# Kernel optimization log

Measured on AMD Instinct MI355X. Metric: run time of the kernel, lower is better.

The kernel has to match this reference:

```python
import jax, jax.numpy as jnp
import numpy as np

N = 50000
E = 800000
IN_DIM = 128
HID = 64


def _glorot(key, shape):
    fan_in, fan_out = shape[0], shape[-1]
    lim = jnp.sqrt(6.0 / (fan_in + fan_out))
    return jax.random.uniform(key, shape, jnp.float32, -lim, lim)


def setup_inputs() -> dict:
    key = jax.random.key(0)
    ks = jax.random.split(key, 12)
    x = jax.random.normal(ks[0], (N, IN_DIM), jnp.float32)
    edge_index = jax.random.randint(ks[1], (2, E), 0, N, jnp.int64)
    return {
        "x": x,
        "edge_index": edge_index,
        # GATConv 1: in=128 -> 64 per head, 4 heads (concat -> 256)
        "W1": _glorot(ks[2], (IN_DIM, 4 * HID)),
        "a_src1": _glorot(ks[3], (4, HID)),
        "a_dst1": _glorot(ks[4], (4, HID)),
        "b1": jnp.zeros((4 * HID,), jnp.float32),
        # GATConv 2: in=256 -> 64, 1 head
        "W2": _glorot(ks[5], (4 * HID, HID)),
        "a_src2": _glorot(ks[6], (1, HID)),
        "a_dst2": _glorot(ks[7], (1, HID)),
        "b2": jnp.zeros((HID,), jnp.float32),
        # classifier 64 -> 32 -> 2
        "W3": _glorot(ks[8], (HID, 32)),
        "b3": jnp.zeros((32,), jnp.float32),
        "W4": _glorot(ks[9], (32, 2)),
        "b4": jnp.zeros((2,), jnp.float32),
    }


def _gat_layer(x, edge_index, W, a_src, a_dst, b, heads, out_ch):
    """PyG-style GATConv (add_self_loops=True, negative_slope=0.2, concat)."""
    n = x.shape[0]
    loop = jnp.arange(n, dtype=edge_index.dtype)
    src = jnp.concatenate([edge_index[0], loop])  # [E+N]
    dst = jnp.concatenate([edge_index[1], loop])
    h = (x @ W).reshape(n, heads, out_ch)  # [N,H,C]
    as_ = jnp.sum(h * a_src[None], axis=-1)  # [N,H]
    ad_ = jnp.sum(h * a_dst[None], axis=-1)  # [N,H]
    e = jax.nn.leaky_relu(as_[src] + ad_[dst], negative_slope=0.2)  # [E+N,H]
    # segment softmax over destination nodes
    m = jax.ops.segment_max(e, dst, num_segments=n)  # [N,H]
    ex = jnp.exp(e - m[dst])
    s = jax.ops.segment_sum(ex, dst, num_segments=n)
    alpha = ex / (s[dst] + 1e-16)  # [E+N,H]
    msg = h[src] * alpha[:, :, None]  # [E+N,H,C]
    out = jax.ops.segment_sum(msg, dst, num_segments=n)  # [N,H,C]
    return out.reshape(n, heads * out_ch) + b


def reference(x, edge_index, W1, a_src1, a_dst1, b1, W2, a_src2, a_dst2, b2, W3, b3, W4, b4):
    h = jax.nn.elu(_gat_layer(x, edge_index, W1, a_src1, a_dst1, b1, heads=4, out_ch=HID))
    h = jax.nn.elu(_gat_layer(h, edge_index, W2, a_src2, a_dst2, b2, heads=1, out_ch=HID))
    h = jax.nn.relu(h @ W3 + b3)
    return h @ W4 + b4  # [N, 2] logits
```

## Files before the change

kernel.cpp:

```cpp
#include <hip/hip_runtime.h>
#include <math.h>

#define NNODES 50000
#define NEDGES 800000
#define CAP 128
#define SB 832

typedef __attribute__((ext_vector_type(8))) short bfrag8;
typedef __attribute__((ext_vector_type(4))) float f32x4;

__device__ __forceinline__ unsigned short f2bf(float f) {
    unsigned b = __float_as_uint(f);
    b += 0x7fffu + ((b >> 16) & 1u);
    return (unsigned short)(b >> 16);
}
__device__ __forceinline__ float bf_lo(unsigned u) { return __uint_as_float(u << 16); }
__device__ __forceinline__ float bf_hi(unsigned u) { return __uint_as_float(u & 0xffff0000u); }

__device__ __forceinline__ void pack_one(const float* W, unsigned short* Wp, int K, int NC,
                                         int idx) {
    int k = idx / NC, n = idx % NC;
    int kf = k >> 5, q = (k >> 3) & 3, j = k & 7;
    Wp[((((size_t)n * (K >> 5) + kf) * 4 + q) << 3) + j] = f2bf(W[idx]);
}

__global__ void prep_kernel(const float* __restrict__ x, unsigned short* __restrict__ xb,
                            const float* __restrict__ W1, unsigned short* __restrict__ W1p,
                            const float* __restrict__ W2, unsigned short* __restrict__ W2p,
                            int* __restrict__ cnt, int ncvt4, int n) {
    int idx = blockIdx.x * blockDim.x + threadIdx.x;
    if (idx < ncvt4) {
        float4 v = *(const float4*)&x[idx * 4];
        ushort4 s;
        s.x = f2bf(v.x); s.y = f2bf(v.y); s.z = f2bf(v.z); s.w = f2bf(v.w);
        *(ushort4*)&xb[idx * 4] = s;
    }
    if (idx < 128 * 256) pack_one(W1, W1p, 128, 256, idx);
    if (idx < 256 * 64) pack_one(W2, W2p, 256, 64, idx);
    if (idx < n) cnt[idx] = 0;
}

template <int K, int H>
__device__ __forceinline__ void gemm_dev(const unsigned short* __restrict__ Ab,
                                         const unsigned short* __restrict__ Bp,
                                         const float* __restrict__ a_src,
                                         const float* __restrict__ a_dst,
                                         unsigned short* __restrict__ Cb,
                                         float* __restrict__ as_, float* __restrict__ ad_,
                                         int M, int bid) {
    constexpr int KF = K / 32;
    constexpr int NC = H * 64;
    int wave = threadIdx.x >> 6, lane = threadIdx.x & 63;
    int m0 = (bid * 4 + wave) * 16;
    if (m0 >= M) return;
    int quad = lane >> 4, l16 = lane & 15;
    int row = m0 + l16;

    bfrag8 a[KF];
    const unsigned short* arow = Ab + (size_t)row * K + quad * 8;
#pragma unroll
    for (int f = 0; f < KF; f++) a[f] = *(const bfrag8*)(arow + f * 32);

    float ps[4] = {0.f, 0.f, 0.f, 0.f};
    float pd[4] = {0.f, 0.f, 0.f, 0.f};
#pragma unroll
    for (int nt = 0; nt < NC / 16; nt++) {
        f32x4 acc = {0.f, 0.f, 0.f, 0.f};
        const unsigned short* bp = Bp + (((size_t)(nt * 16 + l16) * KF) * 4 + quad) * 8;
#pragma unroll
        for (int f = 0; f < KF; f++) {
            bfrag8 bfr = *(const bfrag8*)(bp + (size_t)f * 32);
            acc = __builtin_amdgcn_mfma_f32_16x16x32_bf16(a[f], bfr, acc, 0, 0, 0);
        }
        int col = nt * 16 + l16;
        float avs = a_src[col], avd = a_dst[col];
#pragma unroll
        for (int r = 0; r < 4; r++) {
            ps[r] = fmaf(acc[r], avs, ps[r]);
            pd[r] = fmaf(acc[r], avd, pd[r]);
            unsigned pk = (unsigned)f2bf(acc[r]) |
                          ((unsigned)f2bf(__shfl_down(acc[r], 1)) << 16);
            if (!(l16 & 1))
                *(unsigned*)&Cb[(size_t)(m0 + quad * 4 + r) * NC + nt * 16 + l16] = pk;
        }
        if ((nt & 3) == 3) {
            int head = nt >> 2;
#pragma unroll
            for (int off = 1; off < 16; off <<= 1) {
#pragma unroll
                for (int r = 0; r < 4; r++) {
                    ps[r] += __shfl_xor(ps[r], off);
                    pd[r] += __shfl_xor(pd[r], off);
                }
            }
            if (l16 == 0) {
#pragma unroll
                for (int r = 0; r < 4; r++) {
                    as_[(size_t)(m0 + quad * 4 + r) * H + head] = ps[r];
                    ad_[(size_t)(m0 + quad * 4 + r) * H + head] = pd[r];
                }
            }
#pragma unroll
            for (int r = 0; r < 4; r++) { ps[r] = 0.f; pd[r] = 0.f; }
        }
    }
}

__global__ __launch_bounds__(256) void gemm1_scatter(
    const unsigned short* __restrict__ xb, const unsigned short* __restrict__ W1p,
    const float* __restrict__ a_src1, const float* __restrict__ a_dst1,
    unsigned short* __restrict__ h1b, float* __restrict__ as1, float* __restrict__ ad1,
    const int* __restrict__ ei, int* __restrict__ cnt, unsigned short* __restrict__ bucket,
    int M, int nE, int nT) {
    if ((int)blockIdx.x < SB) {
        int p = blockIdx.x & 7;
        int q = blockIdx.x >> 3;
        const int NQ = SB / 8;
        for (int idx = q * 256 + threadIdx.x; idx < nT; idx += NQ * 256) {
            int dst = (idx < nE) ? ei[nE + idx] : idx - nE;
            if ((dst & 7) != p) continue;
            int src = (idx < nE) ? ei[idx] : dst;
            int slot = atomicAdd(&cnt[dst], 1);
            if (slot < CAP) bucket[(size_t)dst * CAP + slot] = (unsigned short)src;
        }
    } else {
        gemm_dev<128, 4>(xb, W1p, a_src1, a_dst1, h1b, as1, ad1, M, blockIdx.x - SB);
    }
}

__global__ __launch_bounds__(256) void gemm2_kernel(
    const unsigned short* __restrict__ Ab, const unsigned short* __restrict__ Bp,
    const float* __restrict__ a_src, const float* __restrict__ a_dst,
    unsigned short* __restrict__ Cb, float* __restrict__ as_, float* __restrict__ ad_,
    int M) {
    gemm_dev<256, 1>(Ab, Bp, a_src, a_dst, Cb, as_, ad_, M, blockIdx.x);
}

__global__ void node_agg4(const int* __restrict__ cnt, const unsigned short* __restrict__ bucket,
                          const float* __restrict__ as_, const float* __restrict__ ad_,
                          const unsigned short* __restrict__ hb, const float* __restrict__ b,
                          unsigned short* __restrict__ outb, int n) {
    __shared__ float alf[4][64][4];
    __shared__ int srs[4][64];
    int w = threadIdx.x >> 6;
    int node = blockIdx.x * 4 + w;
    int lane = threadIdx.x & 63;
    if (node >= n) return;
    int cntAll = cnt[node];
    if (cntAll > CAP) cntAll = CAP;
    const unsigned short* bkt = bucket + (size_t)node * CAP;
    int cnt0 = cntAll < 64 ? cntAll : 64;
    bool v0 = lane < cnt0;
    int half = lane >> 5;
    int hl = lane & 31;
    int head = hl >> 3;
    int ch0 = hl * 8;

    float4 adv = *(const float4*)&ad_[node * 4];
    float adn[4] = {adv.x, adv.y, adv.z, adv.w};

    int src0 = bkt[v0 ? lane : 0];
    float4 asv = *(const float4*)&as_[src0 * 4];
    float x0[4];
    {
        float e0 = asv.x + adn[0], e1 = asv.y + adn[1];
        float e2 = asv.z + adn[2], e3 = asv.w + adn[3];
        e0 = e0 > 0.f ? e0 : 0.2f * e0;
        e1 = e1 > 0.f ? e1 : 0.2f * e1;
        e2 = e2 > 0.f ? e2 : 0.2f * e2;
        e3 = e3 > 0.f ? e3 : 0.2f * e3;
        x0[0] = v0 ? __expf(e0) : 0.f;
        x0[1] = v0 ? __expf(e1) : 0.f;
        x0[2] = v0 ? __expf(e2) : 0.f;
        x0[3] = v0 ? __expf(e3) : 0.f;
    }
    bool hv2 = false;
    int src2 = 0;
    float x2[4] = {0.f, 0.f, 0.f, 0.f};
    if (cntAll > 64) {
        int i2 = 64 + lane;
        hv2 = i2 < cntAll;
        src2 = bkt[hv2 ? i2 : 0];
        float4 a2 = *(const float4*)&as_[src2 * 4];
        float t0 = a2.x + adn[0], t1 = a2.y + adn[1];
        float t2 = a2.z + adn[2], t3 = a2.w + adn[3];
        t0 = t0 > 0.f ? t0 : 0.2f * t0;
        t1 = t1 > 0.f ? t1 : 0.2f * t1;
        t2 = t2 > 0.f ? t2 : 0.2f * t2;
        t3 = t3 > 0.f ? t3 : 0.2f * t3;
        x2[0] = hv2 ? __expf(t0) : 0.f;
        x2[1] = hv2 ? __expf(t1) : 0.f;
        x2[2] = hv2 ? __expf(t2) : 0.f;
        x2[3] = hv2 ? __expf(t3) : 0.f;
    }
    srs[w][lane] = src0;
    *(float4*)&alf[w][lane][0] = make_float4(x0[0], x0[1], x0[2], x0[3]);

    float acc[8];
#pragma unroll
    for (int k = 0; k < 8; k++) acc[k] = 0.f;

    int iters = (cnt0 + 1) >> 1;
    int iters4 = (iters + 3) & ~3;

#define LD4(vk, ak, t)                                              \
    {                                                               \
        int e_ = 2 * (t) + half;                                    \
        int s_ = srs[w][e_];                                        \
        ak = alf[w][e_][head];                                      \
        vk = *(const uint4*)&hb[(size_t)s_ * 256 + ch0];            \
    }
#define FMA8(ak, vk)                                                \
    {                                                               \
        acc[0] = fmaf(ak, bf_lo(vk.x), acc[0]);                     \
        acc[1] = fmaf(ak, bf_hi(vk.x), acc[1]);                     \
        acc[2] = fmaf(ak, bf_lo(vk.y), acc[2]);                     \
        acc[3] = fmaf(ak, bf_hi(vk.y), acc[3]);                     \
        acc[4] = fmaf(ak, bf_lo(vk.z), acc[4]);                     \
        acc[5] = fmaf(ak, bf_hi(vk.z), acc[5]);                     \
        acc[6] = fmaf(ak, bf_lo(vk.w), acc[6]);                     \
        acc[7] = fmaf(ak, bf_hi(vk.w), acc[7]);                     \
    }

    uint4 q0, q1, q2, q3;
    float a0, a1, a2, a3;
    LD4(q0, a0, 0) LD4(q1, a1, 1) LD4(q2, a2, 2) LD4(q3, a3, 3)
    int c = 0;
    for (; c < iters4 - 4; c += 4) {
        FMA8(a0, q0) LD4(q0, a0, c + 4)
        FMA8(a1, q1) LD4(q1, a1, c + 5)
        FMA8(a2, q2) LD4(q2, a2, c + 6)
        FMA8(a3, q3) LD4(q3, a3, c + 7)
    }
    FMA8(a0, q0) FMA8(a1, q1) FMA8(a2, q2) FMA8(a3, q3)

    if (cntAll > 64) {
        srs[w][lane] = src2;
        *(float4*)&alf[w][lane][0] = make_float4(x2[0], x2[1], x2[2], x2[3]);
        int c2 = cntAll - 64;
        for (int j = 0; j < c2; j += 2) {
            int e_ = j + half;
            int s_ = srs[w][e_];
            float al = alf[w][e_][head];
            uint4 v = *(const uint4*)&hb[(size_t)s_ * 256 + ch0];
            FMA8(al, v)
        }
    }
    float sl[4];
#pragma unroll
    for (int h = 0; h < 4; h++) sl[h] = x0[h] + x2[h];
#pragma unroll
    for (int off = 32; off > 0; off >>= 1) {
#pragma unroll
        for (int h = 0; h < 4; h++) sl[h] += __shfl_xor(sl[h], off);
    }
    float inv_h = 1.f / (sl[head] + 1e-16f);

#pragma unroll
    for (int k = 0; k < 8; k++) acc[k] += __shfl_down(acc[k], 32);
    if (half == 0) {
        float4 b0 = *(const float4*)&b[ch0];
        float4 b1 = *(const float4*)&b[ch0 + 4];
        float o[8] = {fmaf(acc[0], inv_h, b0.x), fmaf(acc[1], inv_h, b0.y),
                      fmaf(acc[2], inv_h, b0.z), fmaf(acc[3], inv_h, b0.w),
                      fmaf(acc[4], inv_h, b1.x), fmaf(acc[5], inv_h, b1.y),
                      fmaf(acc[6], inv_h, b1.z), fmaf(acc[7], inv_h, b1.w)};
#pragma unroll
        for (int k = 0; k < 8; k++) o[k] = o[k] > 0.f ? o[k] : __expf(o[k]) - 1.f;
        uint4 p;
        p.x = f2bf(o[0]) | ((unsigned)f2bf(o[1]) << 16);
        p.y = f2bf(o[2]) | ((unsigned)f2bf(o[3]) << 16);
        p.z = f2bf(o[4]) | ((unsigned)f2bf(o[5]) << 16);
        p.w = f2bf(o[6]) | ((unsigned)f2bf(o[7]) << 16);
        *(uint4*)&outb[(size_t)node * 256 + ch0] = p;
    }
#undef LD4
#undef FMA8
}

__global__ void node_agg1_cls(const int* __restrict__ cnt,
                              const unsigned short* __restrict__ bucket,
                              const float* __restrict__ as_, const float* __restrict__ ad_,
                              const unsigned short* __restrict__ hb,
                              const float* __restrict__ b2v,
                              const float* __restrict__ W3, const float* __restrict__ b3,
                              const float* __restrict__ W4, const float* __restrict__ b4,
                              float* __restrict__ out, int n) {
    __shared__ float alf[4][64];
    __shared__ int srs[4][64];
    __shared__ float w3s[2048];
    __shared__ float w4s[64], b3s[32], b4s[2];
    __shared__ float zrow[4][64];
    __shared__ float hrow[4][32];
    int tid = threadIdx.x;
    int w = tid >> 6;
    int lane = tid & 63;
#pragma unroll
    for (int i = 0; i < 8; i++) w3s[i * 256 + tid] = W3[i * 256 + tid];
    if (tid < 64) w4s[tid] = W4[tid];
    if (tid < 32) b3s[tid] = b3[tid];
    if (tid < 2) b4s[tid] = b4[tid];
    __syncthreads();

    int node = blockIdx.x * 4 + w;
    if (node >= n) return;
    int cntAll = cnt[node];
    if (cntAll > CAP) cntAll = CAP;
    const unsigned short* bkt = bucket + (size_t)node * CAP;
    int cnt0 = cntAll < 64 ? cntAll : 64;
    bool v0 = lane < cnt0;
    int q = lane >> 4;
    int ql = lane & 15;
    int ch0 = ql * 4;

    float adn = ad_[node];
    int src0 = bkt[v0 ? lane : 0];
    float ev = as_[src0] + adn;
    ev = ev > 0.f ? ev : 0.2f * ev;
    float x0 = v0 ? __expf(ev) : 0.f;

    bool hv2 = false;
    int src2 = 0;
    float x2 = 0.f;
    if (cntAll > 64) {
        int i2 = 64 + lane;
        hv2 = i2 < cntAll;
        src2 = bkt[hv2 ? i2 : 0];
        float t = as_[src2] + adn;
        t = t > 0.f ? t : 0.2f * t;
        x2 = hv2 ? __expf(t) : 0.f;
    }
    srs[w][lane] = src0;
    alf[w][lane] = x0;

    float acc[4] = {0.f, 0.f, 0.f, 0.f};
    int iters = (cnt0 + 3) >> 2;
    int iters4 = (iters + 3) & ~3;

#define LD2(vk, ak, t)                                              \
    {                                                               \
        int e_ = 4 * (t) + q;                                       \
        int s_ = srs[w][e_];                                        \
        ak = alf[w][e_];                                            \
        vk = *(const uint2*)&hb[(size_t)s_ * 64 + ch0];             \
    }
#define FMA4(ak, vk)                                                \
    {                                                               \
        acc[0] = fmaf(ak, bf_lo(vk.x), acc[0]);                     \
        acc[1] = fmaf(ak, bf_hi(vk.x), acc[1]);                     \
        acc[2] = fmaf(ak, bf_lo(vk.y), acc[2]);                     \
        acc[3] = fmaf(ak, bf_hi(vk.y), acc[3]);                     \
    }

    uint2 q0, q1, q2, q3;
    float a0, a1, a2, a3;
    LD2(q0, a0, 0) LD2(q1, a1, 1) LD2(q2, a2, 2) LD2(q3, a3, 3)
    int c = 0;
    for (; c < iters4 - 4; c += 4) {
        FMA4(a0, q0) LD2(q0, a0, c + 4)
        FMA4(a1, q1) LD2(q1, a1, c + 5)
        FMA4(a2, q2) LD2(q2, a2, c + 6)
        FMA4(a3, q3) LD2(q3, a3, c + 7)
    }
    FMA4(a0, q0) FMA4(a1, q1) FMA4(a2, q2) FMA4(a3, q3)

    if (cntAll > 64) {
        srs[w][lane] = src2;
        alf[w][lane] = x2;
        int c2 = cntAll - 64;
        for (int j = 0; j < c2; j += 4) {
            int e_ = j + q;
            int s_ = srs[w][e_];
            float al = alf[w][e_];
            uint2 v = *(const uint2*)&hb[(size_t)s_ * 64 + ch0];
            FMA4(al, v)
        }
    }
    float sl = x0 + x2;
#pragma unroll
    for (int off = 32; off > 0; off >>= 1) sl += __shfl_xor(sl, off);
    float inv_s = 1.f / (sl + 1e-16f);

#pragma unroll
    for (int k = 0; k < 4; k++) {
        acc[k] += __shfl_down(acc[k], 32);
        acc[k] += __shfl_down(acc[k], 16);
    }
    if (q == 0) {
        float4 bv = *(const float4*)&b2v[ch0];
        float o0 = fmaf(acc[0], inv_s, bv.x), o1 = fmaf(acc[1], inv_s, bv.y);
        float o2 = fmaf(acc[2], inv_s, bv.z), o3 = fmaf(acc[3], inv_s, bv.w);
        zrow[w][ch0 + 0] = o0 > 0.f ? o0 : __expf(o0) - 1.f;
        zrow[w][ch0 + 1] = o1 > 0.f ? o1 : __expf(o1) - 1.f;
        zrow[w][ch0 + 2] = o2 > 0.f ? o2 : __expf(o2) - 1.f;
        zrow[w][ch0 + 3] = o3 > 0.f ? o3 : __expf(o3) - 1.f;
    }
    {
        int p = lane & 1, j = lane >> 1;
        float partial = 0.f;
#pragma unroll
        for (int i = 0; i < 32; i++) {
            int k = p * 32 + i;
            partial = fmaf(zrow[w][k], w3s[k * 32 + j], partial);
        }
        partial += __shfl_down(partial, 1);
        if (p == 0) {
            float hv = partial + b3s[j];
            hrow[w][j] = hv > 0.f ? hv : 0.f;
        }
    }
    if (lane < 2) {
        float o = b4s[lane];
#pragma unroll
        for (int j = 0; j < 32; j++) o = fmaf(hrow[w][j], w4s[j * 2 + lane], o);
        out[(size_t)node * 2 + lane] = o;
    }
#undef LD2
#undef FMA4
}

extern "C" void kernel_launch(void* const* d_in, const int* in_sizes, int n_in,
                              void* d_out, int out_size, void* d_ws, size_t ws_size,
                              hipStream_t stream) {
    const float* x      = (const float*)d_in[0];
    const int*   ei     = (const int*)d_in[1];
    const float* W1     = (const float*)d_in[2];
    const float* a_src1 = (const float*)d_in[3];
    const float* a_dst1 = (const float*)d_in[4];
    const float* b1     = (const float*)d_in[5];
    const float* W2     = (const float*)d_in[6];
    const float* a_src2 = (const float*)d_in[7];
    const float* a_dst2 = (const float*)d_in[8];
    const float* b2     = (const float*)d_in[9];
    const float* W3     = (const float*)d_in[10];
    const float* b3     = (const float*)d_in[11];
    const float* W4     = (const float*)d_in[12];
    const float* b4     = (const float*)d_in[13];
    float* out = (float*)d_out;

    const int N = NNODES, E = NEDGES, ET = E + N;

    float* ws = (float*)d_ws;
    size_t o = 0;
    float* as1  = ws + o; o += (size_t)N * 4;
    float* ad1  = ws + o; o += (size_t)N * 4;
    unsigned short* h1b   = (unsigned short*)(ws + o); o += (size_t)N * 128;
    unsigned short* h2b   = (unsigned short*)(ws + o); o += (size_t)N * 32;
    unsigned short* out1b = (unsigned short*)(ws + o); o += (size_t)N * 128;
    unsigned short* xb    = (unsigned short*)(ws + o); o += (size_t)N * 64;
    unsigned short* W1p   = (unsigned short*)(ws + o); o += 16384;
    unsigned short* W2p   = (unsigned short*)(ws + o); o += 8192;
    int* cnt    = (int*)(ws + o); o += N;
    unsigned short* bucket = (unsigned short*)(ws + o); o += (size_t)N * CAP / 2;

    dim3 blk(256);

    const int NCVT4 = N * 128 / 4;
    prep_kernel<<<(NCVT4 + 255) / 256, blk, 0, stream>>>(x, xb, W1, W1p, W2, W2p, cnt,
                                                         NCVT4, N);

    const int GB = (N + 63) / 64;
    gemm1_scatter<<<SB + GB, blk, 0, stream>>>(xb, W1p, a_src1, a_dst1, h1b, as1, ad1,
                                               ei, cnt, bucket, N, E, ET);

    node_agg4<<<(N + 3) / 4, blk, 0, stream>>>(cnt, bucket, as1, ad1, h1b, b1, out1b, N);

    gemm2_kernel<<<GB, blk, 0, stream>>>(out1b, W2p, a_src2, a_dst2, h2b, as1, ad1, N);

    node_agg1_cls<<<(N + 3) / 4, blk, 0, stream>>>(cnt, bucket, as1, ad1, h2b, b2, W3, b3,
                                                   W4, b4, out, N);
}
```

Before: 275.8 us.

## Pre-seed self-loops in prep, vectorize edge scatter, deepen aggregation prefetch

Self-loop entries are now written in the prep kernel, with each count set to one, so the scatter loop only handles real edges. The scatter loop reads destination indices as int4 and processes four edges per thread iteration, cutting load instructions and per-edge branching. The aggregation kernels double their software-pipelined gather depth from 4 to 8 outstanding row loads. This raises register pressure and rounds iteration counts up to multiples of 8, adding padded work for low-degree nodes. It also assumes the edge count is divisible by 4.

```diff
diff --git a/kernel.cpp b/kernel.cpp
--- a/kernel.cpp
+++ b/kernel.cpp
@@ -27,7 +27,8 @@
 __global__ void prep_kernel(const float* __restrict__ x, unsigned short* __restrict__ xb,
                             const float* __restrict__ W1, unsigned short* __restrict__ W1p,
                             const float* __restrict__ W2, unsigned short* __restrict__ W2p,
-                            int* __restrict__ cnt, int ncvt4, int n) {
+                            int* __restrict__ cnt, unsigned short* __restrict__ bucket,
+                            int ncvt4, int n) {
     int idx = blockIdx.x * blockDim.x + threadIdx.x;
     if (idx < ncvt4) {
         float4 v = *(const float4*)&x[idx * 4];
@@ -37,7 +38,10 @@
     }
     if (idx < 128 * 256) pack_one(W1, W1p, 128, 256, idx);
     if (idx < 256 * 64) pack_one(W2, W2p, 256, 64, idx);
-    if (idx < n) cnt[idx] = 0;
+    if (idx < n) {
+        cnt[idx] = 1;
+        bucket[(size_t)idx * CAP] = (unsigned short)idx;
+    }
 }
 
 template <int K, int H>
@@ -111,17 +115,32 @@
     const float* __restrict__ a_src1, const float* __restrict__ a_dst1,
     unsigned short* __restrict__ h1b, float* __restrict__ as1, float* __restrict__ ad1,
     const int* __restrict__ ei, int* __restrict__ cnt, unsigned short* __restrict__ bucket,
-    int M, int nE, int nT) {
+    int M, int nE) {
     if ((int)blockIdx.x < SB) {
         int p = blockIdx.x & 7;
-        int q = blockIdx.x >> 3;
+        int qb = blockIdx.x >> 3;
         const int NQ = SB / 8;
-        for (int idx = q * 256 + threadIdx.x; idx < nT; idx += NQ * 256) {
-            int dst = (idx < nE) ? ei[nE + idx] : idx - nE;
-            if ((dst & 7) != p) continue;
-            int src = (idx < nE) ? ei[idx] : dst;
-            int slot = atomicAdd(&cnt[dst], 1);
-            if (slot < CAP) bucket[(size_t)dst * CAP + slot] = (unsigned short)src;
+        const int nV = nE / 4;
+        const int4* dst4 = (const int4*)(ei + nE);
+        for (int v = qb * 256 + threadIdx.x; v < nV; v += NQ * 256) {
+            int4 d = dst4[v];
+            int idx = v * 4;
+            if ((d.x & 7) == p) {
+                int slot = atomicAdd(&cnt[d.x], 1);
+                if (slot < CAP) bucket[(size_t)d.x * CAP + slot] = (unsigned short)ei[idx];
+            }
+            if ((d.y & 7) == p) {
+                int slot = atomicAdd(&cnt[d.y], 1);
+                if (slot < CAP) bucket[(size_t)d.y * CAP + slot] = (unsigned short)ei[idx + 1];
+            }
+            if ((d.z & 7) == p) {
+                int slot = atomicAdd(&cnt[d.z], 1);
+                if (slot < CAP) bucket[(size_t)d.z * CAP + slot] = (unsigned short)ei[idx + 2];
+            }
+            if ((d.w & 7) == p) {
+                int slot = atomicAdd(&cnt[d.w], 1);
+                if (slot < CAP) bucket[(size_t)d.w * CAP + slot] = (unsigned short)ei[idx + 3];
+            }
         }
     } else {
         gemm_dev<128, 4>(xb, W1p, a_src1, a_dst1, h1b, as1, ad1, M, blockIdx.x - SB);
@@ -201,7 +220,7 @@
     for (int k = 0; k < 8; k++) acc[k] = 0.f;
 
     int iters = (cnt0 + 1) >> 1;
-    int iters4 = (iters + 3) & ~3;
+    int iters8 = (iters + 7) & ~7;
 
 #define LD4(vk, ak, t)                                              \
     {                                                               \
@@ -222,17 +241,23 @@
         acc[7] = fmaf(ak, bf_hi(vk.w), acc[7]);                     \
     }
 
-    uint4 q0, q1, q2, q3;
-    float a0, a1, a2, a3;
+    uint4 q0, q1, q2, q3, q4, q5, q6, q7;
+    float a0, a1, a2, a3, a4, a5, a6, a7;
     LD4(q0, a0, 0) LD4(q1, a1, 1) LD4(q2, a2, 2) LD4(q3, a3, 3)
+    LD4(q4, a4, 4) LD4(q5, a5, 5) LD4(q6, a6, 6) LD4(q7, a7, 7)
     int c = 0;
-    for (; c < iters4 - 4; c += 4) {
-        FMA8(a0, q0) LD4(q0, a0, c + 4)
-        FMA8(a1, q1) LD4(q1, a1, c + 5)
-        FMA8(a2, q2) LD4(q2, a2, c + 6)
-        FMA8(a3, q3) LD4(q3, a3, c + 7)
+    for (; c < iters8 - 8; c += 8) {
+        FMA8(a0, q0) LD4(q0, a0, c + 8)
+        FMA8(a1, q1) LD4(q1, a1, c + 9)
+        FMA8(a2, q2) LD4(q2, a2, c + 10)
+        FMA8(a3, q3) LD4(q3, a3, c + 11)
+        FMA8(a4, q4) LD4(q4, a4, c + 12)
+        FMA8(a5, q5) LD4(q5, a5, c + 13)
+        FMA8(a6, q6) LD4(q6, a6, c + 14)
+        FMA8(a7, q7) LD4(q7, a7, c + 15)
     }
     FMA8(a0, q0) FMA8(a1, q1) FMA8(a2, q2) FMA8(a3, q3)
+    FMA8(a4, q4) FMA8(a5, q5) FMA8(a6, q6) FMA8(a7, q7)
 
     if (cntAll > 64) {
         srs[w][lane] = src2;
@@ -335,7 +360,7 @@
 
     float acc[4] = {0.f, 0.f, 0.f, 0.f};
     int iters = (cnt0 + 3) >> 2;
-    int iters4 = (iters + 3) & ~3;
+    int iters8 = (iters + 7) & ~7;
 
 #define LD2(vk, ak, t)                                              \
     {                                                               \
@@ -352,17 +377,23 @@
         acc[3] = fmaf(ak, bf_hi(vk.y), acc[3]);                     \
     }
 
-    uint2 q0, q1, q2, q3;
-    float a0, a1, a2, a3;
+    uint2 q0, q1, q2, q3, q4, q5, q6, q7;
+    float a0, a1, a2, a3, a4, a5, a6, a7;
     LD2(q0, a0, 0) LD2(q1, a1, 1) LD2(q2, a2, 2) LD2(q3, a3, 3)
+    LD2(q4, a4, 4) LD2(q5, a5, 5) LD2(q6, a6, 6) LD2(q7, a7, 7)
     int c = 0;
-    for (; c < iters4 - 4; c += 4) {
-        FMA4(a0, q0) LD2(q0, a0, c + 4)
-        FMA4(a1, q1) LD2(q1, a1, c + 5)
-        FMA4(a2, q2) LD2(q2, a2, c + 6)
-        FMA4(a3, q3) LD2(q3, a3, c + 7)
+    for (; c < iters8 - 8; c += 8) {
+        FMA4(a0, q0) LD2(q0, a0, c + 8)
+        FMA4(a1, q1) LD2(q1, a1, c + 9)
+        FMA4(a2, q2) LD2(q2, a2, c + 10)
+        FMA4(a3, q3) LD2(q3, a3, c + 11)
+        FMA4(a4, q4) LD2(q4, a4, c + 12)
+        FMA4(a5, q5) LD2(q5, a5, c + 13)
+        FMA4(a6, q6) LD2(q6, a6, c + 14)
+        FMA4(a7, q7) LD2(q7, a7, c + 15)
     }
     FMA4(a0, q0) FMA4(a1, q1) FMA4(a2, q2) FMA4(a3, q3)
+    FMA4(a4, q4) FMA4(a5, q5) FMA4(a6, q6) FMA4(a7, q7)
 
     if (cntAll > 64) {
         srs[w][lane] = src2;
@@ -438,7 +469,7 @@
     const float* b4     = (const float*)d_in[13];
     float* out = (float*)d_out;
 
-    const int N = NNODES, E = NEDGES, ET = E + N;
+    const int N = NNODES, E = NEDGES;
 
     float* ws = (float*)d_ws;
     size_t o = 0;
@@ -457,11 +488,11 @@
 
     const int NCVT4 = N * 128 / 4;
     prep_kernel<<<(NCVT4 + 255) / 256, blk, 0, stream>>>(x, xb, W1, W1p, W2, W2p, cnt,
-                                                         NCVT4, N);
+                                                         bucket, NCVT4, N);
 
     const int GB = (N + 63) / 64;
     gemm1_scatter<<<SB + GB, blk, 0, stream>>>(xb, W1p, a_src1, a_dst1, h1b, as1, ad1,
-                                               ei, cnt, bucket, N, E, ET);
+                                               ei, cnt, bucket, N, E);
 
     node_agg4<<<(N + 3) / 4, blk, 0, stream>>>(cnt, bucket, as1, ad1, h1b, b1, out1b, N);
 
```

New measurement: 284.6 us. +3.2%, slower.
